# Kernel tuning notes

Measured on AMD Instinct MI355X. Metric: run time of the kernel, lower is better.

## Reference

```python
import jax, jax.numpy as jnp
import numpy as np

N_NODES = 50000
N_EDGES = 800000
N_GRAPHS = 512
EPS = 1e-5
SLOPE = 0.2  # LeakyReLU negative slope in GATv2


def setup_inputs() -> dict:
    key = jax.random.key(0)
    ks = jax.random.split(key, 20)
    s = 0.1
    inp = {
        "x": jax.random.normal(ks[0], (N_NODES, 9), jnp.float32),
        "edge_attr": jax.random.normal(ks[1], (N_EDGES, 3), jnp.float32),
        "Wl0": jax.random.normal(ks[2], (9, 64), jnp.float32) * s,
        "Wr0": jax.random.normal(ks[3], (9, 64), jnp.float32) * s,
        "bl0": jnp.zeros((64,), jnp.float32),
        "br0": jnp.zeros((64,), jnp.float32),
        "We0": jax.random.normal(ks[4], (3, 64), jnp.float32) * s,
        "att0": jax.random.normal(ks[5], (64,), jnp.float32) * s,
        "bo0": jnp.zeros((64,), jnp.float32),
        "Wl": jax.random.normal(ks[6], (4, 64, 64), jnp.float32) * s,
        "Wr": jax.random.normal(ks[7], (4, 64, 64), jnp.float32) * s,
        "bl": jnp.zeros((4, 64), jnp.float32),
        "br": jnp.zeros((4, 64), jnp.float32),
        "We": jax.random.normal(ks[8], (4, 3, 64), jnp.float32) * s,
        "att": jax.random.normal(ks[9], (4, 64), jnp.float32) * s,
        "bo": jnp.zeros((4, 64), jnp.float32),
        "bn_g": jnp.ones((5, 64), jnp.float32),
        "bn_b": jnp.zeros((5, 64), jnp.float32),
        "bn_m": jnp.zeros((5, 64), jnp.float32),
        "bn_v": jax.random.uniform(ks[10], (5, 64), jnp.float32, 0.5, 1.5),
        "Wjk": jax.random.normal(ks[11], (64, 64), jnp.float32) * s,
        "bjk": jnp.zeros((64,), jnp.float32),
        "Whead": jax.random.normal(ks[12], (64, 1), jnp.float32) * s,
        "bhead": jnp.zeros((1,), jnp.float32),
        "edge_index": jax.random.randint(ks[13], (2, N_EDGES), 0, N_NODES, jnp.int32),
        "batch": jnp.sort(jax.random.randint(ks[14], (N_NODES,), 0, N_GRAPHS, jnp.int32)),
        "num_graphs": N_GRAPHS,
    }
    return inp


def gatv2_layer(h, src, dst, ea, Wl_, bl_, Wr_, br_, We_, a_, bo_, n_nodes):
    # GATv2Conv (heads=1, edge_dim) : e_ij = a . LeakyReLU(Wl h_j + Wr h_i + We e_ij)
    xl = h @ Wl_ + bl_                          # [N, 64] source transform
    xr = h @ Wr_ + br_                          # [N, 64] dest transform
    e = jax.nn.leaky_relu(xl[src] + xr[dst] + ea @ We_, SLOPE)  # [E, 64]
    logit = e @ a_                              # [E]
    m = jax.ops.segment_max(logit, dst, num_segments=n_nodes)
    m = jnp.where(jnp.isfinite(m), m, 0.0)      # empty segments -> -inf
    p = jnp.exp(logit - m[dst])
    z = jax.ops.segment_sum(p, dst, num_segments=n_nodes)
    alpha = p / jnp.maximum(z[dst], 1e-16)      # softmax over in-edges of dst
    out = jax.ops.segment_sum(alpha[:, None] * xl[src], dst, num_segments=n_nodes)
    return out + bo_


def bn_relu(h, g, b, m, v):
    # eval-mode BatchNorm1d followed by ReLU (BasicGNN: norm then act)
    return jax.nn.relu((h - m) * (g * jax.lax.rsqrt(v + EPS)) + b)


def reference(x, edge_attr, Wl0, Wr0, bl0, br0, We0, att0, bo0,
              Wl, Wr, bl, br, We, att, bo,
              bn_g, bn_b, bn_m, bn_v, Wjk, bjk, Whead, bhead,
              edge_index, batch, num_graphs):
    n = x.shape[0]
    src, dst = edge_index[0], edge_index[1]
    h = gatv2_layer(x, src, dst, edge_attr, Wl0, bl0, Wr0, br0, We0, att0, bo0, n)
    h = bn_relu(h, bn_g[0], bn_b[0], bn_m[0], bn_v[0])
    for i in range(4):
        h = gatv2_layer(h, src, dst, edge_attr, Wl[i], bl[i], Wr[i], br[i], We[i], att[i], bo[i], n)
        h = bn_relu(h, bn_g[i + 1], bn_b[i + 1], bn_m[i + 1], bn_v[i + 1])
    h = h @ Wjk + bjk                            # jk='last' output projection 64->64
    # global mean pool over graphs
    sums = jax.ops.segment_sum(h, batch, num_segments=num_graphs)          # [G, 64]
    cnt = jax.ops.segment_sum(jnp.ones((n,), h.dtype), batch, num_segments=num_graphs)
    pooled = sums / jnp.maximum(cnt, 1.0)[:, None]
    return pooled @ Whead + bhead                # [G, 1]  (dropout inactive in eval)
```

## Files before the change

kernel.cpp:

```cpp
#include <hip/hip_runtime.h>
#include <math.h>

#define N_NODES 50000
#define N_EDGES 800000
#define N_GRAPHS 512
#define SLOPE 0.2f
#define CAP 48
static constexpr float EPS_BN = 1e-5f;

typedef float v2f __attribute__((ext_vector_type(2)));


__global__ __launch_bounds__(256) void scatter_t9_kernel(
    const int* __restrict__ src, const int* __restrict__ dst,
    const float* __restrict__ ea,
    int* __restrict__ cnt, float4* __restrict__ rec,
    const float* __restrict__ x,
    const float* __restrict__ Wl0, const float* __restrict__ bl0,
    const float* __restrict__ Wr0, const float* __restrict__ br0,
    float* __restrict__ xl, float* __restrict__ xr) {
    int t = threadIdx.x;
    int e = blockIdx.x * 256 + t;
    if (e < N_EDGES) {
        int d = dst[e];
        int pos = atomicAdd(&cnt[d], 1);
        if (pos < CAP)
            rec[(size_t)d * CAP + pos] = make_float4(__int_as_float(src[e] * 64),
                                                     ea[e * 3 + 0], ea[e * 3 + 1], ea[e * 3 + 2]);
    }

    int w = t >> 6;
    int k = t & 63;
    v2f wlr[9];
#pragma unroll
    for (int j = 0; j < 9; j++) wlr[j] = (v2f){Wl0[j * 64 + k], Wr0[j * 64 + k]};
    v2f bias = {bl0[k], br0[k]};
    const int NW = gridDim.x * 4;
    for (int n = blockIdx.x * 4 + w; n < N_NODES; n += NW) {
        int un = __builtin_amdgcn_readfirstlane(n);
        const float* __restrict__ hrow = x + (size_t)un * 9;
        float hb[9];
#pragma unroll
        for (int j = 0; j < 9; j++) hb[j] = hrow[j];
        v2f acc = bias;
#pragma unroll
        for (int j = 0; j < 9; j++)
            acc = __builtin_elementwise_fma((v2f){hb[j], hb[j]}, wlr[j], acc);
        xl[(size_t)un * 64 + k] = acc.x;
        xr[(size_t)un * 64 + k] = acc.y;
    }
}


__global__ __launch_bounds__(256) void transform6_kernel(
    const float* __restrict__ h,
    const float* __restrict__ Wl, const float* __restrict__ bl,
    const float* __restrict__ Wr, const float* __restrict__ br,
    float* __restrict__ xl, float* __restrict__ xr) {
    __shared__ float sAt[64][68];
    __shared__ float sB[64][128];
    int t = threadIdx.x;
    int n0 = blockIdx.x * 64;

#pragma unroll
    for (int i = 0; i < 4; i++) {
        int idx = i * 256 + t;
        int row = idx >> 4;
        int fc  = idx & 15;
        int n = n0 + row;
        float4 v = (n < N_NODES) ? *((const float4*)(h + (size_t)n * 64 + fc * 4))
                                 : make_float4(0.f, 0.f, 0.f, 0.f);
        sAt[fc * 4 + 0][row] = v.x;
        sAt[fc * 4 + 1][row] = v.y;
        sAt[fc * 4 + 2][row] = v.z;
        sAt[fc * 4 + 3][row] = v.w;
    }
#pragma unroll
    for (int i = 0; i < 8; i++) {
        int idx = i * 256 + t;
        int j  = idx >> 5;
        int fc = idx & 31;
        int c  = fc * 4;
        float4 v = (c < 64) ? *((const float4*)(Wl + j * 64 + c))
                            : *((const float4*)(Wr + j * 64 + (c - 64)));
        *((float4*)&sB[j][c]) = v;
    }
    __syncthreads();

    int tx = t & 15, ty = t >> 4;
    int c0 = tx * 4;
    float4 bls = *((const float4*)(bl + c0));
    float4 brs = *((const float4*)(br + c0));
    v2f acc[4][4];
#pragma unroll
    for (int r = 0; r < 4; r++) {
        acc[r][0] = (v2f){bls.x, bls.y};
        acc[r][1] = (v2f){bls.z, bls.w};
        acc[r][2] = (v2f){brs.x, brs.y};
        acc[r][3] = (v2f){brs.z, brs.w};
    }

#pragma unroll 4
    for (int j = 0; j < 64; j++) {
        float a0 = sAt[j][ty * 4 + 0];
        float a1 = sAt[j][ty * 4 + 1];
        float a2 = sAt[j][ty * 4 + 2];
        float a3 = sAt[j][ty * 4 + 3];
        float4 bq0 = *((const float4*)&sB[j][c0]);
        float4 bq1 = *((const float4*)&sB[j][64 + c0]);
        v2f b0 = {bq0.x, bq0.y}, b1 = {bq0.z, bq0.w};
        v2f b2 = {bq1.x, bq1.y}, b3 = {bq1.z, bq1.w};
        v2f a0v = {a0, a0}, a1v = {a1, a1}, a2v = {a2, a2}, a3v = {a3, a3};
        acc[0][0] = __builtin_elementwise_fma(a0v, b0, acc[0][0]);
        acc[0][1] = __builtin_elementwise_fma(a0v, b1, acc[0][1]);
        acc[0][2] = __builtin_elementwise_fma(a0v, b2, acc[0][2]);
        acc[0][3] = __builtin_elementwise_fma(a0v, b3, acc[0][3]);
        acc[1][0] = __builtin_elementwise_fma(a1v, b0, acc[1][0]);
        acc[1][1] = __builtin_elementwise_fma(a1v, b1, acc[1][1]);
        acc[1][2] = __builtin_elementwise_fma(a1v, b2, acc[1][2]);
        acc[1][3] = __builtin_elementwise_fma(a1v, b3, acc[1][3]);
        acc[2][0] = __builtin_elementwise_fma(a2v, b0, acc[2][0]);
        acc[2][1] = __builtin_elementwise_fma(a2v, b1, acc[2][1]);
        acc[2][2] = __builtin_elementwise_fma(a2v, b2, acc[2][2]);
        acc[2][3] = __builtin_elementwise_fma(a2v, b3, acc[2][3]);
        acc[3][0] = __builtin_elementwise_fma(a3v, b0, acc[3][0]);
        acc[3][1] = __builtin_elementwise_fma(a3v, b1, acc[3][1]);
        acc[3][2] = __builtin_elementwise_fma(a3v, b2, acc[3][2]);
        acc[3][3] = __builtin_elementwise_fma(a3v, b3, acc[3][3]);
    }

#pragma unroll
    for (int r = 0; r < 4; r++) {
        int n = n0 + ty * 4 + r;
        if (n < N_NODES) {
            *((float4*)(xl + (size_t)n * 64 + c0)) =
                make_float4(acc[r][0].x, acc[r][0].y, acc[r][1].x, acc[r][1].y);
            *((float4*)(xr + (size_t)n * 64 + c0)) =
                make_float4(acc[r][2].x, acc[r][2].y, acc[r][3].x, acc[r][3].y);
        }
    }
}


#define EDGE_T(rX, xXa, xXb, accX)                                        \
    {                                                                     \
        v2f tXa = xXa + xra, tXb = xXb + xrb;                             \
        tXa = __builtin_elementwise_fma((v2f){rX.y, rX.y}, we0a, tXa);    \
        tXb = __builtin_elementwise_fma((v2f){rX.y, rX.y}, we0b, tXb);    \
        tXa = __builtin_elementwise_fma((v2f){rX.z, rX.z}, we1a, tXa);    \
        tXb = __builtin_elementwise_fma((v2f){rX.z, rX.z}, we1b, tXb);    \
        tXa = __builtin_elementwise_fma((v2f){rX.w, rX.w}, we2a, tXa);    \
        tXb = __builtin_elementwise_fma((v2f){rX.w, rX.w}, we2b, tXb);    \
        tXa = __builtin_elementwise_max(tXa, tXa * SLOPE);                \
        tXb = __builtin_elementwise_max(tXb, tXb * SLOPE);                \
        v2f dX = ata * tXa;                                               \
        dX = __builtin_elementwise_fma(atb, tXb, dX);                     \
        accX = dX.x + dX.y;                                               \
    }

__global__ __launch_bounds__(256) void gat_fused11_kernel(
    const float* __restrict__ xl, const float* __restrict__ xr,
    const float4* __restrict__ recP, const int* __restrict__ cnt,
    const float* __restrict__ We, const float* __restrict__ att,
    const float* __restrict__ bo,
    const float* __restrict__ bn_g, const float* __restrict__ bn_b,
    const float* __restrict__ bn_m, const float* __restrict__ bn_v,
    float* __restrict__ hout) {
    int t = threadIdx.x;
    int w = t >> 6;
    int lane = t & 63;
    int q = lane >> 4;
    int r = lane & 15;
    int k4 = r * 4;

    float4 we0 = *(const float4*)(We + 0 * 64 + k4);
    float4 we1 = *(const float4*)(We + 64 + k4);
    float4 we2 = *(const float4*)(We + 128 + k4);
    float4 at4 = *(const float4*)(att + k4);
    v2f we0a = {we0.x, we0.y}, we0b = {we0.z, we0.w};
    v2f we1a = {we1.x, we1.y}, we1b = {we1.z, we1.w};
    v2f we2a = {we2.x, we2.y}, we2b = {we2.z, we2.w};
    v2f ata  = {at4.x, at4.y}, atb  = {at4.z, at4.w};
    float4 bo4 = *(const float4*)(bo + k4);
    float4 g4  = *(const float4*)(bn_g + k4);
    float4 b4  = *(const float4*)(bn_b + k4);
    float4 m4  = *(const float4*)(bn_m + k4);
    float4 v4  = *(const float4*)(bn_v + k4);
    float4 S, C;
    S.x = g4.x / sqrtf(v4.x + EPS_BN);  C.x = (bo4.x - m4.x) * S.x + b4.x;
    S.y = g4.y / sqrtf(v4.y + EPS_BN);  C.y = (bo4.y - m4.y) * S.y + b4.y;
    S.z = g4.z / sqrtf(v4.z + EPS_BN);  C.z = (bo4.z - m4.z) * S.z + b4.z;
    S.w = g4.w / sqrtf(v4.w + EPS_BN);  C.w = (bo4.w - m4.w) * S.w + b4.w;

    const int NW = gridDim.x * 4;
    for (int n0 = blockIdx.x * 4 + w; n0 < N_NODES; n0 += NW) {
        int n = __builtin_amdgcn_readfirstlane(n0);
        float4 xq = *(const float4*)(xr + (size_t)n * 64 + k4);
        v2f xra = {xq.x, xq.y}, xrb = {xq.z, xq.w};
        int beg = n * CAP;
        int end = beg + min(cnt[n], CAP);

        v2f oAa = {0.f, 0.f}, oAb = {0.f, 0.f};
        v2f oBa = {0.f, 0.f}, oBb = {0.f, 0.f};
        float zA = 0.f, zB = 0.f;

        int c = beg;
        int pA0 = c + q;      bool vA0 = pA0 < end;
        int pB0 = c + 4 + q;  bool vB0 = pB0 < end;
        float4 rA0 = recP[vA0 ? pA0 : beg];
        float4 rB0 = recP[vB0 ? pB0 : beg];
        int pA1 = c + 8 + q;  bool vA1 = pA1 < end;
        int pB1 = c + 12 + q; bool vB1 = pB1 < end;
        float4 rA1 = recP[vA1 ? pA1 : beg];
        float4 rB1 = recP[vB1 ? pB1 : beg];
        float4 xA0 = *(const float4*)(xl + ((unsigned)__float_as_int(rA0.x) + k4));
        float4 xB0 = *(const float4*)(xl + ((unsigned)__float_as_int(rB0.x) + k4));

        while (c < end) {
            float4 xA1 = *(const float4*)(xl + ((unsigned)__float_as_int(rA1.x) + k4));
            float4 xB1 = *(const float4*)(xl + ((unsigned)__float_as_int(rB1.x) + k4));
            int c2 = c + 16;
            int pA2 = c2 + q;     bool vA2 = pA2 < end;
            int pB2 = c2 + 4 + q; bool vB2 = pB2 < end;
            float4 rA2 = recP[vA2 ? pA2 : beg];
            float4 rB2 = recP[vB2 ? pB2 : beg];

            v2f xAa = {xA0.x, xA0.y}, xAb = {xA0.z, xA0.w};
            v2f xBa = {xB0.x, xB0.y}, xBb = {xB0.z, xB0.w};

            float accA, accB;
            EDGE_T(rA0, xAa, xAb, accA);
            EDGE_T(rB0, xBa, xBb, accB);

            accA += __shfl_xor(accA, 1, 64);  accB += __shfl_xor(accB, 1, 64);
            accA += __shfl_xor(accA, 2, 64);  accB += __shfl_xor(accB, 2, 64);
            accA += __shfl_xor(accA, 4, 64);  accB += __shfl_xor(accB, 4, 64);
            accA += __shfl_xor(accA, 8, 64);  accB += __shfl_xor(accB, 8, 64);

            float peA = vA0 ? __expf(accA) : 0.f;
            float peB = vB0 ? __expf(accB) : 0.f;
            v2f pAv = {peA, peA}, pBv = {peB, peB};
            oAa = __builtin_elementwise_fma(pAv, xAa, oAa);
            oAb = __builtin_elementwise_fma(pAv, xAb, oAb);
            oBa = __builtin_elementwise_fma(pBv, xBa, oBa);
            oBb = __builtin_elementwise_fma(pBv, xBb, oBb);
            zA += peA; zB += peB;

            rA0 = rA1; rB0 = rB1; vA0 = vA1; vB0 = vB1;
            rA1 = rA2; rB1 = rB2; vA1 = vA2; vB1 = vB2;
            xA0 = xA1; xB0 = xB1;
            c += 8;
        }

        v2f oa = oAa + oBa, ob = oAb + oBb;
        float z = zA + zB;
        float4 o = make_float4(oa.x, oa.y, ob.x, ob.y);
        o.x += __shfl_xor(o.x, 16, 64); o.x += __shfl_xor(o.x, 32, 64);
        o.y += __shfl_xor(o.y, 16, 64); o.y += __shfl_xor(o.y, 32, 64);
        o.z += __shfl_xor(o.z, 16, 64); o.z += __shfl_xor(o.z, 32, 64);
        o.w += __shfl_xor(o.w, 16, 64); o.w += __shfl_xor(o.w, 32, 64);
        z += __shfl_xor(z, 16, 64); z += __shfl_xor(z, 32, 64);

        if (q == 0) {
            float zi = 1.0f / fmaxf(z, 1e-16f);
            float4 res;
            res.x = fmaxf(fmaf(o.x * zi, S.x, C.x), 0.f);
            res.y = fmaxf(fmaf(o.y * zi, S.y, C.y), 0.f);
            res.z = fmaxf(fmaf(o.z * zi, S.z, C.z), 0.f);
            res.w = fmaxf(fmaf(o.w * zi, S.w, C.w), 0.f);
            *(float4*)(hout + (size_t)n * 64 + k4) = res;
        }
    }
}


__global__ __launch_bounds__(256) void pool_all2_kernel(
    const float* __restrict__ h, const int* __restrict__ batch,
    const float* __restrict__ Wjk, const float* __restrict__ bjk,
    const float* __restrict__ Whead, const float* __restrict__ bhead,
    float* __restrict__ out) {
    __shared__ float red[4][64];
    int g = blockIdx.x;
    int t = threadIdx.x;
    int k = t & 63;
    int w = t >> 6;
    int lo = 0, hi = N_NODES;
    while (lo < hi) { int mid = (lo + hi) >> 1; if (batch[mid] < g) lo = mid + 1; else hi = mid; }
    int s = lo;
    hi = N_NODES;
    while (lo < hi) { int mid = (lo + hi) >> 1; if (batch[mid] < g + 1) lo = mid + 1; else hi = mid; }
    int e = lo;

    float acc = 0.f;
    for (int n = s + w; n < e; n += 4) acc += h[(size_t)n * 64 + k];
    red[w][k] = acc;
    __syncthreads();

    if (w == 0) {
        acc = (red[0][k] + red[1][k]) + (red[2][k] + red[3][k]);
        float wc = 0.f;
        for (int j = 0; j < 64; j++) wc = fmaf(Wjk[k * 64 + j], Whead[j], wc);
        float bc = bjk[k] * Whead[k];
        for (int off = 32; off > 0; off >>= 1) bc += __shfl_xor(bc, off, 64);
        float cntf = (float)(e - s);
        acc /= fmaxf(cntf, 1.0f);
        float v = acc * wc;
        for (int off = 32; off > 0; off >>= 1) v += __shfl_xor(v, off, 64);
        if (k == 0) out[g] = v + bc + bhead[0];
    }
}


extern "C" void kernel_launch(void* const* d_in, const int* in_sizes, int n_in,
                              void* d_out, int out_size, void* d_ws, size_t ws_size,
                              hipStream_t stream) {
    const float* x     = (const float*)d_in[0];
    const float* ea    = (const float*)d_in[1];
    const float* Wl0   = (const float*)d_in[2];
    const float* Wr0   = (const float*)d_in[3];
    const float* bl0   = (const float*)d_in[4];
    const float* br0   = (const float*)d_in[5];
    const float* We0   = (const float*)d_in[6];
    const float* att0  = (const float*)d_in[7];
    const float* bo0   = (const float*)d_in[8];
    const float* Wl    = (const float*)d_in[9];
    const float* Wr    = (const float*)d_in[10];
    const float* bl    = (const float*)d_in[11];
    const float* br    = (const float*)d_in[12];
    const float* We    = (const float*)d_in[13];
    const float* att   = (const float*)d_in[14];
    const float* bo    = (const float*)d_in[15];
    const float* bn_g  = (const float*)d_in[16];
    const float* bn_b  = (const float*)d_in[17];
    const float* bn_m  = (const float*)d_in[18];
    const float* bn_v  = (const float*)d_in[19];
    const float* Wjk   = (const float*)d_in[20];
    const float* bjk   = (const float*)d_in[21];
    const float* Whead = (const float*)d_in[22];
    const float* bhead = (const float*)d_in[23];
    const int* edge_index = (const int*)d_in[24];
    const int* batch      = (const int*)d_in[25];

    const int* srcIdx = edge_index;
    const int* dstIdx = edge_index + N_EDGES;

    char* ws = (char*)d_ws;
    size_t off = 0;
    auto alloc = [&](size_t bytes) -> void* {
        void* p = ws + off;
        off += (bytes + 255) & ~(size_t)255;
        return p;
    };
    float* hA      = (float*)alloc((size_t)N_NODES * 64 * 4);
    float* hB      = (float*)alloc((size_t)N_NODES * 64 * 4);
    float* xlb     = (float*)alloc((size_t)N_NODES * 64 * 4);
    float* xrb     = (float*)alloc((size_t)N_NODES * 64 * 4);
    int*   cnt     = (int*)alloc((size_t)N_NODES * 4);
    float4* recP   = (float4*)alloc((size_t)N_NODES * CAP * 16);

    hipMemsetAsync(cnt, 0, (size_t)N_NODES * 4, stream);
    scatter_t9_kernel<<<(N_EDGES + 255) / 256, 256, 0, stream>>>(
        srcIdx, dstIdx, ea, cnt, recP, x, Wl0, bl0, Wr0, br0, xlb, xrb);

    const int GB  = 2048;
    const int NBG = (N_NODES + 63) / 64;

    gat_fused11_kernel<<<GB, 256, 0, stream>>>(xlb, xrb, recP, cnt,
                                               We0, att0, bo0,
                                               bn_g, bn_b, bn_m, bn_v, hA);

    float* hcur = hA;
    float* hnext = hB;
    for (int i = 0; i < 4; i++) {
        transform6_kernel<<<NBG, 256, 0, stream>>>(hcur,
            Wl + (size_t)i * 64 * 64, bl + (size_t)i * 64,
            Wr + (size_t)i * 64 * 64, br + (size_t)i * 64,
            xlb, xrb);
        gat_fused11_kernel<<<GB, 256, 0, stream>>>(xlb, xrb, recP, cnt,
            We + (size_t)i * 3 * 64, att + (size_t)i * 64,
            bo + (size_t)i * 64,
            bn_g + (size_t)(i + 1) * 64, bn_b + (size_t)(i + 1) * 64,
            bn_m + (size_t)(i + 1) * 64, bn_v + (size_t)(i + 1) * 64,
            hnext);
        float* tp = hcur; hcur = hnext; hnext = tp;
    }

    pool_all2_kernel<<<N_GRAPHS, 256, 0, stream>>>(hcur, batch, Wjk, bjk, Whead, bhead,
                                                   (float*)d_out);
}
```

Before: 447.9 us.

## Fuse next-layer Wl/Wr transform into GAT aggregation kernel

```diff
diff --git a/kernel.cpp b/kernel.cpp
--- a/kernel.cpp
+++ b/kernel.cpp
@@ -7,6 +7,7 @@
 #define SLOPE 0.2f
 #define CAP 48
 static constexpr float EPS_BN = 1e-5f;
+static constexpr unsigned MAXOFF = (N_NODES - 1) * 64;
 
 typedef float v2f __attribute__((ext_vector_type(2)));
 
@@ -52,96 +53,6 @@
 }
 
 
-__global__ __launch_bounds__(256) void transform6_kernel(
-    const float* __restrict__ h,
-    const float* __restrict__ Wl, const float* __restrict__ bl,
-    const float* __restrict__ Wr, const float* __restrict__ br,
-    float* __restrict__ xl, float* __restrict__ xr) {
-    __shared__ float sAt[64][68];
-    __shared__ float sB[64][128];
-    int t = threadIdx.x;
-    int n0 = blockIdx.x * 64;
-
-#pragma unroll
-    for (int i = 0; i < 4; i++) {
-        int idx = i * 256 + t;
-        int row = idx >> 4;
-        int fc  = idx & 15;
-        int n = n0 + row;
-        float4 v = (n < N_NODES) ? *((const float4*)(h + (size_t)n * 64 + fc * 4))
-                                 : make_float4(0.f, 0.f, 0.f, 0.f);
-        sAt[fc * 4 + 0][row] = v.x;
-        sAt[fc * 4 + 1][row] = v.y;
-        sAt[fc * 4 + 2][row] = v.z;
-        sAt[fc * 4 + 3][row] = v.w;
-    }
-#pragma unroll
-    for (int i = 0; i < 8; i++) {
-        int idx = i * 256 + t;
-        int j  = idx >> 5;
-        int fc = idx & 31;
-        int c  = fc * 4;
-        float4 v = (c < 64) ? *((const float4*)(Wl + j * 64 + c))
-                            : *((const float4*)(Wr + j * 64 + (c - 64)));
-        *((float4*)&sB[j][c]) = v;
-    }
-    __syncthreads();
-
-    int tx = t & 15, ty = t >> 4;
-    int c0 = tx * 4;
-    float4 bls = *((const float4*)(bl + c0));
-    float4 brs = *((const float4*)(br + c0));
-    v2f acc[4][4];
-#pragma unroll
-    for (int r = 0; r < 4; r++) {
-        acc[r][0] = (v2f){bls.x, bls.y};
-        acc[r][1] = (v2f){bls.z, bls.w};
-        acc[r][2] = (v2f){brs.x, brs.y};
-        acc[r][3] = (v2f){brs.z, brs.w};
-    }
-
-#pragma unroll 4
-    for (int j = 0; j < 64; j++) {
-        float a0 = sAt[j][ty * 4 + 0];
-        float a1 = sAt[j][ty * 4 + 1];
-        float a2 = sAt[j][ty * 4 + 2];
-        float a3 = sAt[j][ty * 4 + 3];
-        float4 bq0 = *((const float4*)&sB[j][c0]);
-        float4 bq1 = *((const float4*)&sB[j][64 + c0]);
-        v2f b0 = {bq0.x, bq0.y}, b1 = {bq0.z, bq0.w};
-        v2f b2 = {bq1.x, bq1.y}, b3 = {bq1.z, bq1.w};
-        v2f a0v = {a0, a0}, a1v = {a1, a1}, a2v = {a2, a2}, a3v = {a3, a3};
-        acc[0][0] = __builtin_elementwise_fma(a0v, b0, acc[0][0]);
-        acc[0][1] = __builtin_elementwise_fma(a0v, b1, acc[0][1]);
-        acc[0][2] = __builtin_elementwise_fma(a0v, b2, acc[0][2]);
-        acc[0][3] = __builtin_elementwise_fma(a0v, b3, acc[0][3]);
-        acc[1][0] = __builtin_elementwise_fma(a1v, b0, acc[1][0]);
-        acc[1][1] = __builtin_elementwise_fma(a1v, b1, acc[1][1]);
-        acc[1][2] = __builtin_elementwise_fma(a1v, b2, acc[1][2]);
-        acc[1][3] = __builtin_elementwise_fma(a1v, b3, acc[1][3]);
-        acc[2][0] = __builtin_elementwise_fma(a2v, b0, acc[2][0]);
-        acc[2][1] = __builtin_elementwise_fma(a2v, b1, acc[2][1]);
-        acc[2][2] = __builtin_elementwise_fma(a2v, b2, acc[2][2]);
-        acc[2][3] = __builtin_elementwise_fma(a2v, b3, acc[2][3]);
-        acc[3][0] = __builtin_elementwise_fma(a3v, b0, acc[3][0]);
-        acc[3][1] = __builtin_elementwise_fma(a3v, b1, acc[3][1]);
-        acc[3][2] = __builtin_elementwise_fma(a3v, b2, acc[3][2]);
-        acc[3][3] = __builtin_elementwise_fma(a3v, b3, acc[3][3]);
-    }
-
-#pragma unroll
-    for (int r = 0; r < 4; r++) {
-        int n = n0 + ty * 4 + r;
-        if (n < N_NODES) {
-            *((float4*)(xl + (size_t)n * 64 + c0)) =
-                make_float4(acc[r][0].x, acc[r][0].y, acc[r][1].x, acc[r][1].y);
-            *((float4*)(xr + (size_t)n * 64 + c0)) =
-                make_float4(acc[r][2].x, acc[r][2].y, acc[r][3].x, acc[r][3].y);
-        }
-    }
-}
-
-
 #define EDGE_T(rX, xXa, xXb, accX)                                        \
     {                                                                     \
         v2f tXa = xXa + xra, tXb = xXb + xrb;                             \
@@ -158,20 +69,37 @@
         accX = dX.x + dX.y;                                               \
     }
 
-__global__ __launch_bounds__(256) void gat_fused11_kernel(
+#define MMROW(kk, hv)                                                              \
+    acc[kk][0] = __builtin_elementwise_fma((v2f){hv, hv}, w0, acc[kk][0]);         \
+    acc[kk][1] = __builtin_elementwise_fma((v2f){hv, hv}, w1, acc[kk][1]);
+
+__global__ __launch_bounds__(256) void gat_fusedT_kernel(
     const float* __restrict__ xl, const float* __restrict__ xr,
     const float4* __restrict__ recP, const int* __restrict__ cnt,
     const float* __restrict__ We, const float* __restrict__ att,
     const float* __restrict__ bo,
     const float* __restrict__ bn_g, const float* __restrict__ bn_b,
     const float* __restrict__ bn_m, const float* __restrict__ bn_v,
-    float* __restrict__ hout) {
+    const float* __restrict__ Wln, const float* __restrict__ bln,
+    const float* __restrict__ Wrn, const float* __restrict__ brn,
+    float* __restrict__ xln, float* __restrict__ xrn) {
+    __shared__ float sW[2][64][68];
+    __shared__ float hT[4][64][12];
     int t = threadIdx.x;
     int w = t >> 6;
     int lane = t & 63;
     int q = lane >> 4;
     int r = lane & 15;
     int k4 = r * 4;
+
+    for (int i = t; i < 2048; i += 256) {
+        int mt = i >> 10;
+        int j  = (i >> 4) & 63;
+        int fc = i & 15;
+        const float* Wsrc = mt ? Wrn : Wln;
+        *((float4*)&sW[mt][j][fc * 4]) = *((const float4*)(Wsrc + j * 64 + fc * 4));
+    }
+    __syncthreads();
 
     float4 we0 = *(const float4*)(We + 0 * 64 + k4);
     float4 we1 = *(const float4*)(We + 64 + k4);
@@ -192,6 +120,161 @@
     S.z = g4.z / sqrtf(v4.z + EPS_BN);  C.z = (bo4.z - m4.z) * S.z + b4.z;
     S.w = g4.w / sqrtf(v4.w + EPS_BN);  C.w = (bo4.w - m4.w) * S.w + b4.w;
 
+    const int mat = q >> 1, jh = q & 1;
+
+    const int NW = gridDim.x * 4;
+    for (int b0 = blockIdx.x * 4 + w; b0 < N_NODES; b0 += NW * 8) {
+        int kmax = 0;
+#pragma unroll 1
+        for (int kk = 0; kk < 8; kk++) {
+            int nn = b0 + kk * NW;
+            if (nn >= N_NODES) break;
+            kmax = kk + 1;
+            int n = __builtin_amdgcn_readfirstlane(nn);
+            int beg = n * CAP;
+            int end = beg + min(cnt[n], CAP);
+            float4 xq = *(const float4*)(xr + (size_t)n * 64 + k4);
+            v2f xra = {xq.x, xq.y}, xrb = {xq.z, xq.w};
+
+            float4 cA0 = recP[beg + q];
+            float4 cB0 = recP[beg + 4 + q];
+            float4 cA1 = recP[beg + 8 + q];
+            float4 cB1 = recP[beg + 12 + q];
+            bool wA0 = (beg + q) < end,      wB0 = (beg + 4 + q) < end;
+            bool wA1 = (beg + 8 + q) < end,  wB1 = (beg + 12 + q) < end;
+            float4 gA0 = *(const float4*)(xl + (min((unsigned)__float_as_int(cA0.x), MAXOFF) + k4));
+            float4 gB0 = *(const float4*)(xl + (min((unsigned)__float_as_int(cB0.x), MAXOFF) + k4));
+
+            v2f oAa = {0.f, 0.f}, oAb = {0.f, 0.f};
+            v2f oBa = {0.f, 0.f}, oBb = {0.f, 0.f};
+            float zA = 0.f, zB = 0.f;
+
+            int c = beg;
+            while (c < end) {
+                float4 gA1 = *(const float4*)(xl + (min((unsigned)__float_as_int(cA1.x), MAXOFF) + k4));
+                float4 gB1 = *(const float4*)(xl + (min((unsigned)__float_as_int(cB1.x), MAXOFF) + k4));
+                float4 cA2 = recP[c + 16 + q];
+                float4 cB2 = recP[c + 20 + q];
+                bool wA2 = (c + 16 + q) < end, wB2 = (c + 20 + q) < end;
+
+                v2f xAa = {gA0.x, gA0.y}, xAb = {gA0.z, gA0.w};
+                v2f xBa = {gB0.x, gB0.y}, xBb = {gB0.z, gB0.w};
+
+                float accA, accB;
+                EDGE_T(cA0, xAa, xAb, accA);
+                EDGE_T(cB0, xBa, xBb, accB);
+
+                accA += __shfl_xor(accA, 1, 64);  accB += __shfl_xor(accB, 1, 64);
+                accA += __shfl_xor(accA, 2, 64);  accB += __shfl_xor(accB, 2, 64);
+                accA += __shfl_xor(accA, 4, 64);  accB += __shfl_xor(accB, 4, 64);
+                accA += __shfl_xor(accA, 8, 64);  accB += __shfl_xor(accB, 8, 64);
+
+                float peA = wA0 ? __expf(accA) : 0.f;
+                float peB = wB0 ? __expf(accB) : 0.f;
+                v2f pAv = {peA, peA}, pBv = {peB, peB};
+                oAa = __builtin_elementwise_fma(pAv, xAa, oAa);
+                oAb = __builtin_elementwise_fma(pAv, xAb, oAb);
+                oBa = __builtin_elementwise_fma(pBv, xBa, oBa);
+                oBb = __builtin_elementwise_fma(pBv, xBb, oBb);
+                zA += peA; zB += peB;
+
+                cA0 = cA1; cB0 = cB1; wA0 = wA1; wB0 = wB1;
+                cA1 = cA2; cB1 = cB2; wA1 = wA2; wB1 = wB2;
+                gA0 = gA1; gB0 = gB1;
+                c += 8;
+            }
+
+            v2f oa = oAa + oBa, ob = oAb + oBb;
+            float z = zA + zB;
+            float4 o = make_float4(oa.x, oa.y, ob.x, ob.y);
+            o.x += __shfl_xor(o.x, 16, 64); o.x += __shfl_xor(o.x, 32, 64);
+            o.y += __shfl_xor(o.y, 16, 64); o.y += __shfl_xor(o.y, 32, 64);
+            o.z += __shfl_xor(o.z, 16, 64); o.z += __shfl_xor(o.z, 32, 64);
+            o.w += __shfl_xor(o.w, 16, 64); o.w += __shfl_xor(o.w, 32, 64);
+            z += __shfl_xor(z, 16, 64); z += __shfl_xor(z, 32, 64);
+
+            if (q == 0) {
+                float zi = 1.0f / fmaxf(z, 1e-16f);
+                hT[w][k4 + 0][kk] = fmaxf(fmaf(o.x * zi, S.x, C.x), 0.f);
+                hT[w][k4 + 1][kk] = fmaxf(fmaf(o.y * zi, S.y, C.y), 0.f);
+                hT[w][k4 + 2][kk] = fmaxf(fmaf(o.z * zi, S.z, C.z), 0.f);
+                hT[w][k4 + 3][kk] = fmaxf(fmaf(o.w * zi, S.w, C.w), 0.f);
+            }
+        }
+
+        asm volatile("s_waitcnt lgkmcnt(0)" ::: "memory");
+
+        v2f acc[8][2];
+#pragma unroll
+        for (int kk = 0; kk < 8; kk++) { acc[kk][0] = (v2f){0.f, 0.f}; acc[kk][1] = (v2f){0.f, 0.f}; }
+#pragma unroll 4
+        for (int j16 = 0; j16 < 32; j16++) {
+            int j = jh * 32 + j16;
+            float4 wv  = *(const float4*)&sW[mat][j][k4];
+            float4 h03 = *(const float4*)&hT[w][j][0];
+            float4 h47 = *(const float4*)&hT[w][j][4];
+            v2f w0 = {wv.x, wv.y}, w1 = {wv.z, wv.w};
+            MMROW(0, h03.x); MMROW(1, h03.y); MMROW(2, h03.z); MMROW(3, h03.w);
+            MMROW(4, h47.x); MMROW(5, h47.y); MMROW(6, h47.z); MMROW(7, h47.w);
+        }
+#pragma unroll
+        for (int kk = 0; kk < 8; kk++) {
+            acc[kk][0].x += __shfl_xor(acc[kk][0].x, 16, 64);
+            acc[kk][0].y += __shfl_xor(acc[kk][0].y, 16, 64);
+            acc[kk][1].x += __shfl_xor(acc[kk][1].x, 16, 64);
+            acc[kk][1].y += __shfl_xor(acc[kk][1].y, 16, 64);
+        }
+        if (jh == 0) {
+            float* dstp = mat ? xrn : xln;
+            float4 be = mat ? *(const float4*)(brn + k4) : *(const float4*)(bln + k4);
+#pragma unroll
+            for (int kk = 0; kk < 8; kk++) {
+                if (kk < kmax) {
+                    int nn = b0 + kk * NW;
+                    float4 o4 = make_float4(acc[kk][0].x + be.x, acc[kk][0].y + be.y,
+                                            acc[kk][1].x + be.z, acc[kk][1].y + be.w);
+                    *((float4*)(dstp + (size_t)nn * 64 + k4)) = o4;
+                }
+            }
+        }
+    }
+}
+
+
+__global__ __launch_bounds__(256) void gat_fused12_kernel(
+    const float* __restrict__ xl, const float* __restrict__ xr,
+    const float4* __restrict__ recP, const int* __restrict__ cnt,
+    const float* __restrict__ We, const float* __restrict__ att,
+    const float* __restrict__ bo,
+    const float* __restrict__ bn_g, const float* __restrict__ bn_b,
+    const float* __restrict__ bn_m, const float* __restrict__ bn_v,
+    float* __restrict__ hout) {
+    int t = threadIdx.x;
+    int w = t >> 6;
+    int lane = t & 63;
+    int q = lane >> 4;
+    int r = lane & 15;
+    int k4 = r * 4;
+
+    float4 we0 = *(const float4*)(We + 0 * 64 + k4);
+    float4 we1 = *(const float4*)(We + 64 + k4);
+    float4 we2 = *(const float4*)(We + 128 + k4);
+    float4 at4 = *(const float4*)(att + k4);
+    v2f we0a = {we0.x, we0.y}, we0b = {we0.z, we0.w};
+    v2f we1a = {we1.x, we1.y}, we1b = {we1.z, we1.w};
+    v2f we2a = {we2.x, we2.y}, we2b = {we2.z, we2.w};
+    v2f ata  = {at4.x, at4.y}, atb  = {at4.z, at4.w};
+    float4 bo4 = *(const float4*)(bo + k4);
+    float4 g4  = *(const float4*)(bn_g + k4);
+    float4 b4  = *(const float4*)(bn_b + k4);
+    float4 m4  = *(const float4*)(bn_m + k4);
+    float4 v4  = *(const float4*)(bn_v + k4);
+    float4 S, C;
+    S.x = g4.x / sqrtf(v4.x + EPS_BN);  C.x = (bo4.x - m4.x) * S.x + b4.x;
+    S.y = g4.y / sqrtf(v4.y + EPS_BN);  C.y = (bo4.y - m4.y) * S.y + b4.y;
+    S.z = g4.z / sqrtf(v4.z + EPS_BN);  C.z = (bo4.z - m4.z) * S.z + b4.z;
+    S.w = g4.w / sqrtf(v4.w + EPS_BN);  C.w = (bo4.w - m4.w) * S.w + b4.w;
+
     const int NW = gridDim.x * 4;
     for (int n0 = blockIdx.x * 4 + w; n0 < N_NODES; n0 += NW) {
         int n = __builtin_amdgcn_readfirstlane(n0);
@@ -200,45 +283,41 @@
         int beg = n * CAP;
         int end = beg + min(cnt[n], CAP);
 
+        float4 cA0 = recP[beg + q];
+        float4 cB0 = recP[beg + 4 + q];
+        float4 cA1 = recP[beg + 8 + q];
+        float4 cB1 = recP[beg + 12 + q];
+        bool wA0 = (beg + q) < end,      wB0 = (beg + 4 + q) < end;
+        bool wA1 = (beg + 8 + q) < end,  wB1 = (beg + 12 + q) < end;
+        float4 gA0 = *(const float4*)(xl + (min((unsigned)__float_as_int(cA0.x), MAXOFF) + k4));
+        float4 gB0 = *(const float4*)(xl + (min((unsigned)__float_as_int(cB0.x), MAXOFF) + k4));
+
         v2f oAa = {0.f, 0.f}, oAb = {0.f, 0.f};
         v2f oBa = {0.f, 0.f}, oBb = {0.f, 0.f};
         float zA = 0.f, zB = 0.f;
 
         int c = beg;
-        int pA0 = c + q;      bool vA0 = pA0 < end;
-        int pB0 = c + 4 + q;  bool vB0 = pB0 < end;
-        float4 rA0 = recP[vA0 ? pA0 : beg];
-        float4 rB0 = recP[vB0 ? pB0 : beg];
-        int pA1 = c + 8 + q;  bool vA1 = pA1 < end;
-        int pB1 = c + 12 + q; bool vB1 = pB1 < end;
-        float4 rA1 = recP[vA1 ? pA1 : beg];
-        float4 rB1 = recP[vB1 ? pB1 : beg];
-        float4 xA0 = *(const float4*)(xl + ((unsigned)__float_as_int(rA0.x) + k4));
-        float4 xB0 = *(const float4*)(xl + ((unsigned)__float_as_int(rB0.x) + k4));
-
         while (c < end) {
-            float4 xA1 = *(const float4*)(xl + ((unsigned)__float_as_int(rA1.x) + k4));
-            float4 xB1 = *(const float4*)(xl + ((unsigned)__float_as_int(rB1.x) + k4));
-            int c2 = c + 16;
-            int pA2 = c2 + q;     bool vA2 = pA2 < end;
-            int pB2 = c2 + 4 + q; bool vB2 = pB2 < end;
-            float4 rA2 = recP[vA2 ? pA2 : beg];
-            float4 rB2 = recP[vB2 ? pB2 : beg];
-
-            v2f xAa = {xA0.x, xA0.y}, xAb = {xA0.z, xA0.w};
-            v2f xBa = {xB0.x, xB0.y}, xBb = {xB0.z, xB0.w};
+            float4 gA1 = *(const float4*)(xl + (min((unsigned)__float_as_int(cA1.x), MAXOFF) + k4));
+            float4 gB1 = *(const float4*)(xl + (min((unsigned)__float_as_int(cB1.x), MAXOFF) + k4));
+            float4 cA2 = recP[c + 16 + q];
+            float4 cB2 = recP[c + 20 + q];
+            bool wA2 = (c + 16 + q) < end, wB2 = (c + 20 + q) < end;
+
+            v2f xAa = {gA0.x, gA0.y}, xAb = {gA0.z, gA0.w};
+            v2f xBa = {gB0.x, gB0.y}, xBb = {gB0.z, gB0.w};
 
             float accA, accB;
-            EDGE_T(rA0, xAa, xAb, accA);
-            EDGE_T(rB0, xBa, xBb, accB);
+            EDGE_T(cA0, xAa, xAb, accA);
+            EDGE_T(cB0, xBa, xBb, accB);
 
             accA += __shfl_xor(accA, 1, 64);  accB += __shfl_xor(accB, 1, 64);
             accA += __shfl_xor(accA, 2, 64);  accB += __shfl_xor(accB, 2, 64);
             accA += __shfl_xor(accA, 4, 64);  accB += __shfl_xor(accB, 4, 64);
             accA += __shfl_xor(accA, 8, 64);  accB += __shfl_xor(accB, 8, 64);
 
-            float peA = vA0 ? __expf(accA) : 0.f;
-            float peB = vB0 ? __expf(accB) : 0.f;
+            float peA = wA0 ? __expf(accA) : 0.f;
+            float peB = wB0 ? __expf(accB) : 0.f;
             v2f pAv = {peA, peA}, pBv = {peB, peB};
             oAa = __builtin_elementwise_fma(pAv, xAa, oAa);
             oAb = __builtin_elementwise_fma(pAv, xAb, oAb);
@@ -246,9 +325,9 @@
             oBb = __builtin_elementwise_fma(pBv, xBb, oBb);
             zA += peA; zB += peB;
 
-            rA0 = rA1; rB0 = rB1; vA0 = vA1; vB0 = vB1;
-            rA1 = rA2; rB1 = rB2; vA1 = vA2; vB1 = vB2;
-            xA0 = xA1; xB0 = xB1;
+            cA0 = cA1; cB0 = cB1; wA0 = wA1; wB0 = wB1;
+            cA1 = cA2; cB1 = cB2; wA1 = wA2; wB1 = wB2;
+            gA0 = gA1; gB0 = gB1;
             c += 8;
         }
 
@@ -351,40 +430,45 @@
         off += (bytes + 255) & ~(size_t)255;
         return p;
     };
-    float* hA      = (float*)alloc((size_t)N_NODES * 64 * 4);
-    float* hB      = (float*)alloc((size_t)N_NODES * 64 * 4);
-    float* xlb     = (float*)alloc((size_t)N_NODES * 64 * 4);
-    float* xrb     = (float*)alloc((size_t)N_NODES * 64 * 4);
+    float* hbuf    = (float*)alloc((size_t)N_NODES * 64 * 4);
+    float* xlA     = (float*)alloc((size_t)N_NODES * 64 * 4);
+    float* xrA     = (float*)alloc((size_t)N_NODES * 64 * 4);
+    float* xlB     = (float*)alloc((size_t)N_NODES * 64 * 4);
+    float* xrB     = (float*)alloc((size_t)N_NODES * 64 * 4);
     int*   cnt     = (int*)alloc((size_t)N_NODES * 4);
-    float4* recP   = (float4*)alloc((size_t)N_NODES * CAP * 16);
+    float4* recP   = (float4*)alloc(((size_t)N_NODES * CAP + 16) * 16);
 
     hipMemsetAsync(cnt, 0, (size_t)N_NODES * 4, stream);
     scatter_t9_kernel<<<(N_EDGES + 255) / 256, 256, 0, stream>>>(
-        srcIdx, dstIdx, ea, cnt, recP, x, Wl0, bl0, Wr0, br0, xlb, xrb);
-
+        srcIdx, dstIdx, ea, cnt, recP, x, Wl0, bl0, Wr0, br0, xlA, xrA);
+
+    const int GBF = 768;
     const int GB  = 2048;
-    const int NBG = (N_NODES + 63) / 64;
-
-    gat_fused11_kernel<<<GB, 256, 0, stream>>>(xlb, xrb, recP, cnt,
-                                               We0, att0, bo0,
-                                               bn_g, bn_b, bn_m, bn_v, hA);
-
-    float* hcur = hA;
-    float* hnext = hB;
-    for (int i = 0; i < 4; i++) {
-        transform6_kernel<<<NBG, 256, 0, stream>>>(hcur,
+
+    gat_fusedT_kernel<<<GBF, 256, 0, stream>>>(xlA, xrA, recP, cnt,
+        We0, att0, bo0, bn_g, bn_b, bn_m, bn_v,
+        Wl, bl, Wr, br, xlB, xrB);
+    for (int i = 1; i < 4; i++) {
+        const float* xin  = (i & 1) ? xlB : xlA;
+        const float* xrin = (i & 1) ? xrB : xrA;
+        float* xout  = (i & 1) ? xlA : xlB;
+        float* xrout = (i & 1) ? xrA : xrB;
+        gat_fusedT_kernel<<<GBF, 256, 0, stream>>>(xin, xrin, recP, cnt,
+            We + (size_t)(i - 1) * 3 * 64, att + (size_t)(i - 1) * 64,
+            bo + (size_t)(i - 1) * 64,
+            bn_g + (size_t)i * 64, bn_b + (size_t)i * 64,
+            bn_m + (size_t)i * 64, bn_v + (size_t)i * 64,
             Wl + (size_t)i * 64 * 64, bl + (size_t)i * 64,
             Wr + (size_t)i * 64 * 64, br + (size_t)i * 64,
-            xlb, xrb);
-        gat_fused11_kernel<<<GB, 256, 0, stream>>>(xlb, xrb, recP, cnt,
-            We + (size_t)i * 3 * 64, att + (size_t)i * 64,
-            bo + (size_t)i * 64,
-            bn_g + (size_t)(i + 1) * 64, bn_b + (size_t)(i + 1) * 64,
-            bn_m + (size_t)(i + 1) * 64, bn_v + (size_t)(i + 1) * 64,
-            hnext);
-        float* tp = hcur; hcur = hnext; hnext = tp;
-    }
-
-    pool_all2_kernel<<<N_GRAPHS, 256, 0, stream>>>(hcur, batch, Wjk, bjk, Whead, bhead,
+            xout, xrout);
+    }
+
+    gat_fused12_kernel<<<GB, 256, 0, stream>>>(xlA, xrA, recP, cnt,
+        We + (size_t)3 * 3 * 64, att + (size_t)3 * 64, bo + (size_t)3 * 64,
+        bn_g + (size_t)4 * 64, bn_b + (size_t)4 * 64,
+        bn_m + (size_t)4 * 64, bn_v + (size_t)4 * 64,
+        hbuf);
+
+    pool_all2_kernel<<<N_GRAPHS, 256, 0, stream>>>(hbuf, batch, Wjk, bjk, Whead, bhead,
                                                    (float*)d_out);
 }
```

Result: no change. 451.2 us (+0.7%).
